# Optimization experiments

Hardware: AMD Instinct MI355X
Metric: run time of the kernel (lower is better)

The kernel has to match this reference:

```python
import jax, jax.numpy as jnp
import numpy as np

B, S, D, H = 2, 2048, 1024, 16
HD = D // H  # 64
ROPE_BASE = 10000.0


def setup_inputs() -> dict:
    key = jax.random.key(0)
    k1, k2, k3 = jax.random.split(key, 3)
    std = 1.0 / np.sqrt(D)
    x = jax.random.normal(k1, (B, S, D), dtype=jnp.float32)
    w_in = jax.random.normal(k2, (3 * D, D), dtype=jnp.float32) * std
    w_out = jax.random.normal(k3, (D, D), dtype=jnp.float32) * (std / np.sqrt(2.0))
    return {"x": x, "w_in": w_in, "w_out": w_out}


def _rope_cos_sin(seq_len, head_dim):
    inv_freq = 1.0 / (ROPE_BASE ** (jnp.arange(0, head_dim, 2, dtype=jnp.float32) / head_dim))
    t = jnp.arange(seq_len, dtype=jnp.float32)
    freqs = jnp.einsum("s,d->sd", t, inv_freq)          # [S, HD/2]
    emb = jnp.concatenate([freqs, freqs], axis=-1)       # [S, HD]
    return jnp.cos(emb)[None, :, None, :], jnp.sin(emb)[None, :, None, :]


def _rotate_half(x):
    x1, x2 = jnp.split(x, 2, axis=-1)
    return jnp.concatenate([-x2, x1], axis=-1)


def _apply_rope(x, cos, sin):
    return x * cos + _rotate_half(x) * sin


def reference(x, w_in, w_out):
    b, s, d = x.shape
    # fused QKV projection (no bias)
    qkv = x @ w_in.T                                      # [B, S, 3D]
    q, k, v = jnp.split(qkv, 3, axis=-1)
    q = q.reshape(b, s, H, HD)
    k = k.reshape(b, s, H, HD)
    v = v.reshape(b, s, H, HD)
    # rotary (offset = 0, no KV cache)
    cos, sin = _rope_cos_sin(s, HD)
    q = _apply_rope(q, cos, sin)
    k = _apply_rope(k, cos, sin)
    # causal SDPA, scale 1/sqrt(head_dim)
    scale = 1.0 / jnp.sqrt(jnp.asarray(HD, dtype=x.dtype))
    scores = jnp.einsum("bqhd,bkhd->bhqk", q, k) * scale  # [B, H, S, S]
    causal = jnp.tril(jnp.ones((s, s), dtype=bool))
    scores = jnp.where(causal, scores, jnp.asarray(-jnp.inf, dtype=scores.dtype))
    attn = jax.nn.softmax(scores, axis=-1)
    out = jnp.einsum("bhqk,bkhd->bqhd", attn, v).reshape(b, s, d)
    return out @ w_out.T
```

## Files before the change

kernel.cpp:

```cpp
#include <hip/hip_runtime.h>
#include <hip/hip_bf16.h>
#include <math.h>

#define NB 2
#define NS 2048
#define ND 1024
#define NH 16
#define HD 64
#define BS (NB*NS)
#define D3 (3*ND)
#define NT (NS/64)

typedef __bf16 bf16;
typedef __bf16 bf16x4 __attribute__((ext_vector_type(4)));
typedef __bf16 bf16x8 __attribute__((ext_vector_type(8)));
typedef float f32x4 __attribute__((ext_vector_type(4)));

#define MFMA16(a,b,c) __builtin_amdgcn_mfma_f32_16x16x32_bf16(a,b,c,0,0,0)

static __device__ inline f32x4 zero4() { f32x4 z; z[0]=0.f; z[1]=0.f; z[2]=0.f; z[3]=0.f; return z; }

__device__ __forceinline__ void gload_lds16(const bf16* g, bf16* l) {
    __builtin_amdgcn_global_load_lds(
        (__attribute__((address_space(1))) unsigned int*)g,
        (__attribute__((address_space(3))) unsigned int*)l, 16, 0, 0);
}

#define CVT1 (BS*ND/8)
#define CVT2 (D3*ND/8)
#define CVT3 (ND*ND/8)
#define CVTN (CVT1+CVT2+CVT3)
__global__ __launch_bounds__(256) void prep(
    const float* __restrict__ x, const float* __restrict__ w_in, const float* __restrict__ w_out,
    bf16* __restrict__ xb, bf16* __restrict__ winb, bf16* __restrict__ woutb,
    float2* __restrict__ csT)
{
    int i = blockIdx.x * 256 + threadIdx.x;
    if (i < CVTN) {
        const float* in; bf16* out; int j;
        if (i < CVT1)            { in = x;     out = xb;    j = i; }
        else if (i < CVT1+CVT2)  { in = w_in;  out = winb;  j = i - CVT1; }
        else                     { in = w_out; out = woutb; j = i - CVT1 - CVT2; }
        const float4* p = (const float4*)in;
        float4 a = p[j*2], b = p[j*2+1];
        bf16x8 o;
        o[0]=(bf16)a.x; o[1]=(bf16)a.y; o[2]=(bf16)a.z; o[3]=(bf16)a.w;
        o[4]=(bf16)b.x; o[5]=(bf16)b.y; o[6]=(bf16)b.z; o[7]=(bf16)b.w;
        ((bf16x8*)out)[j] = o;
    } else {
        int k = i - CVTN;
        int s = k >> 5, j = k & 31;
        float inv = __expf(-(float)j * (9.210340372f * 0.03125f));
        float ang = (float)s * inv;
        csT[k] = make_float2(cosf(ang), sinf(ang));
    }
}

template<int EPI>
__global__ __launch_bounds__(256) void gemm_bt(
    const bf16* __restrict__ A, const bf16* __restrict__ Bm,
    float* __restrict__ C, bf16* __restrict__ Qb, bf16* __restrict__ Kb, bf16* __restrict__ Vt,
    const float2* __restrict__ csT,
    int M, int N, int K)
{
    __shared__ bf16 As[2][128*64];
    __shared__ bf16 Bs[2][128*64];
    int t = threadIdx.x;
    int lane = t & 63, w = t >> 6;
    int wr = w >> 1, wc = w & 1;
    int lr = lane & 15, lg = lane >> 4;
    int m0 = blockIdx.y * 128, n0 = blockIdx.x * 128;

    int srow = lane >> 3;
    int schunk = (lane & 7) ^ srow;
    const bf16* gA = &A [(size_t)(m0 + w*32 + srow)*K + schunk*8];
    const bf16* gB = &Bm[(size_t)(n0 + w*32 + srow)*K + schunk*8];

    auto stage = [&](int kt) {
        int buf = kt & 1;
        bf16* lA = &As[buf][w*2048];
        bf16* lB = &Bs[buf][w*2048];
        int k0 = kt * 64;
        #pragma unroll
        for (int i=0;i<4;i++) {
            gload_lds16(gA + (size_t)(i*8)*K + k0, lA + i*512);
            gload_lds16(gB + (size_t)(i*8)*K + k0, lB + i*512);
        }
    };

    f32x4 acc[4][4];
    for (int m=0;m<4;m++) for (int n=0;n<4;n++) acc[m][n] = zero4();

    int nt = K >> 6;
    stage(0);
    stage(1);

    for (int kt = 0; kt < nt; kt++) {
        int cur = kt & 1;
        if (kt < nt-1) asm volatile("s_waitcnt vmcnt(8)" ::: "memory");
        else           asm volatile("s_waitcnt vmcnt(0)" ::: "memory");
        __builtin_amdgcn_s_barrier();
        __builtin_amdgcn_sched_barrier(0);

        bf16x8 af[2][4], bfr[2][4];
        #pragma unroll
        for (int ks=0;ks<2;ks++) {
            #pragma unroll
            for (int m=0;m<4;m++) {
                int row = wr*64 + m*16 + lr;
                af[ks][m] = *(const bf16x8*)&As[cur][row*64 + (((ks*4+lg) ^ (row&7))*8)];
            }
            #pragma unroll
            for (int n=0;n<4;n++) {
                int row = wc*64 + n*16 + lr;
                bfr[ks][n] = *(const bf16x8*)&Bs[cur][row*64 + (((ks*4+lg) ^ (row&7))*8)];
            }
        }
        asm volatile("s_waitcnt lgkmcnt(0)" ::: "memory");
        __builtin_amdgcn_sched_barrier(0);
        __builtin_amdgcn_s_barrier();
        __builtin_amdgcn_sched_barrier(0);

        if (kt + 2 < nt) stage(kt + 2);

        __builtin_amdgcn_s_setprio(1);
        #pragma unroll
        for (int ks=0;ks<2;ks++)
            #pragma unroll
            for (int m=0;m<4;m++)
                #pragma unroll
                for (int n=0;n<4;n++)
                    acc[m][n] = MFMA16(af[ks][m], bfr[ks][n], acc[m][n]);
        __builtin_amdgcn_s_setprio(0);
    }

    if (EPI == 0) {
        for (int m=0;m<4;m++) for (int n=0;n<4;n++) {
            int grow = m0 + wr*64 + m*16 + lg*4;
            int gcol = n0 + wc*64 + n*16 + lr;
            for (int r=0;r<4;r++)
                C[(size_t)(grow+r) * N + gcol] = acc[m][n][r];
        }
    } else {
        int which = n0 >> 10;
        if (which == 2) {
            for (int m=0;m<4;m++) for (int n=0;n<4;n++) {
                int grow = m0 + wr*64 + m*16 + lg*4;
                int gcol = n0 + wc*64 + n*16 + lr;
                int h = (gcol & 1023) >> 6, d = gcol & 63;
                int b = grow >> 11, s0 = grow & (NS-1);
                int shi = s0 & ~63, j = s0 & 63;
                int kp = ((j>>5)&1)*32 + ((j>>2)&3)*8 + ((j>>4)&1)*4;
                bf16x4 pv;
                for (int r=0;r<4;r++) pv[r] = (bf16)acc[m][n][r];
                *(bf16x4*)&Vt[((size_t)((b*NH + h)*HD + d))*NS + shi + kp] = pv;
            }
        } else {
            const float qs = 0.125f * 1.44269504f;
            bf16* dst = (which == 0) ? Qb : Kb;
            for (int m=0;m<4;m++) {
                int grow = m0 + wr*64 + m*16 + lg*4;
                #pragma unroll
                for (int n=0;n<2;n++) {
                    int gcol = n0 + wc*64 + n*16 + lr;
                    int h = (gcol & 1023) >> 6, j = gcol & 63;
                    #pragma unroll
                    for (int r=0;r<4;r++) {
                        int gm = grow + r;
                        int b = gm >> 11, s = gm & (NS-1);
                        float2 cs = csT[(s<<5)+j];
                        float x1 = acc[m][n][r], x2 = acc[m][n+2][r];
                        float y1 = x1*cs.x - x2*cs.y;
                        float y2 = x2*cs.x + x1*cs.y;
                        if (which == 0) { y1 *= qs; y2 *= qs; }
                        size_t off = ((size_t)((b*NH + h)*NS + s))*HD;
                        dst[off + j]      = (bf16)y1;
                        dst[off + j + 32] = (bf16)y2;
                    }
                }
            }
        }
    }
}

__global__ __launch_bounds__(256, 4) void attn_fwd(
    const bf16* __restrict__ Qb, const bf16* __restrict__ Kb, const bf16* __restrict__ Vp,
    bf16* __restrict__ AO)
{
    __shared__ bf16 Ks[2][64*64];
    __shared__ bf16 Vs[2][64*64];
    int t = threadIdx.x;
    int lane = t & 63, w = t >> 6;
    int lr = lane & 15, lg = lane >> 4;
    int wgid = blockIdx.x;
    int g = wgid >> 5;
    int qt = (g < 8) ? 31 - g : (g < 16) ? g - 8 : (g < 24) ? 39 - g : g - 16;
    int bh = wgid & 31;
    int b = bh >> 4, h = bh & 15;
    size_t base = (size_t)bh * NS * HD;
    int q0 = qt*64 + w*16;

    bf16x8 qf[2];
    #pragma unroll
    for (int c=0;c<2;c++)
        qf[c] = *(const bf16x8*)&Qb[base + (size_t)(q0+lr)*HD + c*32 + lg*8];

    bf16x8 onesf;
    #pragma unroll
    for (int i=0;i<8;i++) onesf[i] = (bf16)1.0f;

    f32x4 o[4];
    f32x4 lacc = zero4();
    #pragma unroll
    for (int n=0;n<4;n++) o[n] = zero4();
    f32x4 minit;
    minit[0] = -12.f; minit[1] = -12.f; minit[2] = -12.f; minit[3] = -12.f;

    int srow8 = lane >> 3;
    int schunk = (lane & 7) ^ srow8;
    int srcrow = w*8 + srow8;
    const bf16* gK = Kb + base + (size_t)srcrow*HD + schunk*8;
    const bf16* gV = Vp + base + (size_t)srcrow*NS + schunk*8;

    auto stage = [&](int kt) {
        int buf = kt & 1;
        int kv0 = kt * 64;
        #pragma unroll
        for (int i=0;i<2;i++) {
            gload_lds16(gK + (size_t)(kv0 + i*32)*HD, &Ks[buf][(i*32 + w*8)*64]);
            gload_lds16(gV + (size_t)(i*32)*NS + kv0, &Vs[buf][(i*32 + w*8)*64]);
        }
    };

    stage(0);
    if (qt > 0) stage(1);

    for (int kt = 0; kt <= qt; kt++) {
        int cur = kt & 1;
        bool last = (kt == qt);
        if (!last) asm volatile("s_waitcnt vmcnt(4)" ::: "memory");
        else       asm volatile("s_waitcnt vmcnt(0)" ::: "memory");
        __builtin_amdgcn_s_barrier();
        __builtin_amdgcn_sched_barrier(0);

        const bf16* ksb = &Ks[cur][0];
        const bf16* vsb = &Vs[cur][0];

        bf16x8 kf[4][2], vf[2][4];
        #pragma unroll
        for (int kb=0;kb<4;kb++) {
            int row = kb*16 + lr;
            kf[kb][0] = *(const bf16x8*)&ksb[row*64 + ((lg     ^ (row&7))*8)];
            kf[kb][1] = *(const bf16x8*)&ksb[row*64 + (((4+lg) ^ (row&7))*8)];
        }
        #pragma unroll
        for (int c=0;c<2;c++)
            #pragma unroll
            for (int n=0;n<4;n++) {
                int row = n*16 + lr;
                vf[c][n] = *(const bf16x8*)&vsb[row*64 + (((c*4+lg) ^ (row&7))*8)];
            }

        f32x4 sc[4];
        __builtin_amdgcn_s_setprio(1);
        #pragma unroll
        for (int kb=0;kb<4;kb++) {
            sc[kb] = MFMA16(kf[kb][0], qf[0], minit);
            sc[kb] = MFMA16(kf[kb][1], qf[1], sc[kb]);
        }
        __builtin_amdgcn_s_setprio(0);

        if (last) {
            int qi = q0 + lr;
            #pragma unroll
            for (int kb=0;kb<4;kb++)
                #pragma unroll
                for (int rr=0;rr<4;rr++)
                    if (kt*64 + kb*16 + lg*4 + rr > qi) sc[kb][rr] = -__builtin_inff();
        }

        bf16x8 pa[2];
        #pragma unroll
        for (int c=0;c<2;c++) {
            bf16x8 v;
            #pragma unroll
            for (int i=0;i<8;i++) v[i] = (bf16)exp2f(sc[c*2 + (i>>2)][i&3]);
            pa[c] = v;
        }

        asm volatile("s_waitcnt lgkmcnt(0)" ::: "memory");
        __builtin_amdgcn_sched_barrier(0);
        __builtin_amdgcn_s_barrier();
        __builtin_amdgcn_sched_barrier(0);

        if (kt + 2 <= qt) stage(kt + 2);

        __builtin_amdgcn_s_setprio(1);
        #pragma unroll
        for (int c=0;c<2;c++) {
            lacc = MFMA16(onesf, pa[c], lacc);
            #pragma unroll
            for (int n=0;n<4;n++)
                o[n] = MFMA16(vf[c][n], pa[c], o[n]);
        }
        __builtin_amdgcn_s_setprio(0);
    }

    float inv = 1.0f / lacc[0];
    int q = q0 + lr;
    #pragma unroll
    for (int n=0;n<4;n++) {
        bf16x4 ov;
        #pragma unroll
        for (int rr=0;rr<4;rr++) ov[rr] = (bf16)(o[n][rr] * inv);
        *(bf16x4*)&AO[((size_t)(b*NS + q)*NH + h)*HD + n*16 + lg*4] = ov;
    }
}

extern "C" void kernel_launch(void* const* d_in, const int* in_sizes, int n_in,
                              void* d_out, int out_size, void* d_ws, size_t ws_size,
                              hipStream_t stream) {
    const float* x     = (const float*)d_in[0];
    const float* w_in  = (const float*)d_in[1];
    const float* w_out = (const float*)d_in[2];
    float* out = (float*)d_out;

    char* p = (char*)d_ws;
    bf16* xb    = (bf16*)p; p += (size_t)BS*ND*2;
    bf16* winb  = (bf16*)p; p += (size_t)D3*ND*2;
    bf16* woutb = (bf16*)p; p += (size_t)ND*ND*2;
    bf16* Qb    = (bf16*)p; p += (size_t)NB*NH*NS*HD*2;
    bf16* Kb    = (bf16*)p; p += (size_t)NB*NH*NS*HD*2;
    bf16* Vp    = (bf16*)p; p += (size_t)NB*NH*NS*HD*2;
    bf16* AO    = (bf16*)p; p += (size_t)BS*ND*2;
    float2* csT = (float2*)p; p += (size_t)NS*32*8;

    prep<<<(CVTN + NS*32)/256, 256, 0, stream>>>(x, w_in, w_out, xb, winb, woutb, csT);
    gemm_bt<1><<<dim3(D3/128, BS/128), 256, 0, stream>>>(xb, winb, nullptr, Qb, Kb, Vp,
                                                         csT, BS, D3, ND);
    attn_fwd<<<NB*NH*NT, 256, 0, stream>>>(Qb, Kb, Vp, AO);
    gemm_bt<0><<<dim3(ND/128, BS/128), 256, 0, stream>>>(AO, woutb, out, nullptr, nullptr, nullptr,
                                                         nullptr, BS, ND, ND);
}
```

Measured before the change: 96.04 us.

## Use 256x256 eight-wave tile with ping-pong MFMA phases for QKV GEMM

Replaces the 128x128 QKV projection GEMM with a dedicated 512-thread kernel using 256x256 output tiles, so each loaded byte is reused across more MFMAs. The k-loop is split into four quadrant phases with barriers, priority bumps and staggered A/B prefetch, so LDS reads, global-to-LDS loads and MFMAs interleave across waves. The output GEMM is split into its own kernel. The grid for QKV shrinks to 12x16 blocks (192), which may underfill the GPU's compute units and raises register and LDS pressure (64KB LDS per block).

```diff
diff --git a/kernel.cpp b/kernel.cpp
--- a/kernel.cpp
+++ b/kernel.cpp
@@ -56,12 +56,189 @@
     }
 }
 
-template<int EPI>
-__global__ __launch_bounds__(256) void gemm_bt(
+__global__ __launch_bounds__(512, 2) void gemm8_qkv(
     const bf16* __restrict__ A, const bf16* __restrict__ Bm,
-    float* __restrict__ C, bf16* __restrict__ Qb, bf16* __restrict__ Kb, bf16* __restrict__ Vt,
-    const float2* __restrict__ csT,
-    int M, int N, int K)
+    bf16* __restrict__ Qb, bf16* __restrict__ Kb, bf16* __restrict__ Vt,
+    const float2* __restrict__ csT)
+{
+    __shared__ bf16 As[2][256*64];
+    __shared__ bf16 Bs[2][256*64];
+    int t = threadIdx.x;
+    int lane = t & 63, w = t >> 6;
+    int wr = w >> 2, wc = w & 3;
+    int lr = lane & 15, lg = lane >> 4;
+    int m0 = blockIdx.y * 256, n0 = blockIdx.x * 256;
+
+    int srow8 = lane >> 3;
+    int schunk = (lane & 7) ^ srow8;
+    const bf16* gA = A  + (size_t)(m0 + srow8)*ND + schunk*8;
+    const bf16* gB = Bm + (size_t)(n0 + srow8)*ND + schunk*8;
+
+    auto stageA = [&](int kt) {
+        int buf = kt & 1, k0 = kt*64;
+        #pragma unroll
+        for (int i=0;i<2;i++) {
+            int r0 = (w*2+i)*8;
+            gload_lds16(gA + (size_t)r0*ND + k0,       &As[buf][r0*64]);
+            gload_lds16(gA + (size_t)(128+r0)*ND + k0, &As[buf][(128+r0)*64]);
+        }
+    };
+    auto stageB = [&](int kt) {
+        int buf = kt & 1, k0 = kt*64;
+        #pragma unroll
+        for (int i=0;i<2;i++) {
+            int r0 = (w*2+i)*8;
+            gload_lds16(gB + (size_t)r0*ND + k0,       &Bs[buf][r0*64]);
+            gload_lds16(gB + (size_t)(128+r0)*ND + k0, &Bs[buf][(128+r0)*64]);
+        }
+    };
+
+    f32x4 acc[8][4];
+    #pragma unroll
+    for (int m=0;m<8;m++)
+        #pragma unroll
+        for (int n=0;n<4;n++) acc[m][n] = zero4();
+
+    bf16x8 af[4][2], bfr[4][2];
+
+    stageB(0); stageA(0); stageB(1); stageA(1);
+
+    for (int kt = 0; kt < 16; kt++) {
+        int cur = kt & 1;
+        const bf16* as = &As[cur][0];
+        const bf16* bs = &Bs[cur][0];
+        if (kt < 15) asm volatile("s_waitcnt vmcnt(8)" ::: "memory");
+        else         asm volatile("s_waitcnt vmcnt(0)" ::: "memory");
+        __builtin_amdgcn_s_barrier();
+        __builtin_amdgcn_sched_barrier(0);
+
+        #pragma unroll
+        for (int m=0;m<4;m++) {
+            int row = wr*128 + m*16 + lr;
+            af[m][0] = *(const bf16x8*)&as[row*64 + ((lg     ^ (row&7))*8)];
+            af[m][1] = *(const bf16x8*)&as[row*64 + (((4+lg) ^ (row&7))*8)];
+        }
+        #pragma unroll
+        for (int n=0;n<2;n++) {
+            int row = wc*64 + n*16 + lr;
+            bfr[n][0] = *(const bf16x8*)&bs[row*64 + ((lg     ^ (row&7))*8)];
+            bfr[n][1] = *(const bf16x8*)&bs[row*64 + (((4+lg) ^ (row&7))*8)];
+        }
+        asm volatile("s_waitcnt lgkmcnt(0)" ::: "memory");
+        __builtin_amdgcn_sched_barrier(0);
+        __builtin_amdgcn_s_setprio(1);
+        #pragma unroll
+        for (int ks=0;ks<2;ks++)
+            #pragma unroll
+            for (int m=0;m<4;m++)
+                #pragma unroll
+                for (int n=0;n<2;n++)
+                    acc[m][n] = MFMA16(af[m][ks], bfr[n][ks], acc[m][n]);
+        __builtin_amdgcn_s_setprio(0);
+        __builtin_amdgcn_s_barrier();
+        __builtin_amdgcn_sched_barrier(0);
+
+        #pragma unroll
+        for (int n=2;n<4;n++) {
+            int row = wc*64 + n*16 + lr;
+            bfr[n][0] = *(const bf16x8*)&bs[row*64 + ((lg     ^ (row&7))*8)];
+            bfr[n][1] = *(const bf16x8*)&bs[row*64 + (((4+lg) ^ (row&7))*8)];
+        }
+        asm volatile("s_waitcnt lgkmcnt(0)" ::: "memory");
+        __builtin_amdgcn_sched_barrier(0);
+        __builtin_amdgcn_s_setprio(1);
+        #pragma unroll
+        for (int ks=0;ks<2;ks++)
+            #pragma unroll
+            for (int m=0;m<4;m++)
+                #pragma unroll
+                for (int n=2;n<4;n++)
+                    acc[m][n] = MFMA16(af[m][ks], bfr[n][ks], acc[m][n]);
+        __builtin_amdgcn_s_setprio(0);
+        __builtin_amdgcn_s_barrier();
+        __builtin_amdgcn_sched_barrier(0);
+
+        if (kt + 2 < 16) stageB(kt + 2);
+        #pragma unroll
+        for (int m=0;m<4;m++) {
+            int row = wr*128 + (m+4)*16 + lr;
+            af[m][0] = *(const bf16x8*)&as[row*64 + ((lg     ^ (row&7))*8)];
+            af[m][1] = *(const bf16x8*)&as[row*64 + (((4+lg) ^ (row&7))*8)];
+        }
+        asm volatile("s_waitcnt lgkmcnt(0)" ::: "memory");
+        __builtin_amdgcn_sched_barrier(0);
+        __builtin_amdgcn_s_setprio(1);
+        #pragma unroll
+        for (int ks=0;ks<2;ks++)
+            #pragma unroll
+            for (int m=0;m<4;m++)
+                #pragma unroll
+                for (int n=0;n<2;n++)
+                    acc[m+4][n] = MFMA16(af[m][ks], bfr[n][ks], acc[m+4][n]);
+        __builtin_amdgcn_s_setprio(0);
+        __builtin_amdgcn_s_barrier();
+        __builtin_amdgcn_sched_barrier(0);
+
+        if (kt + 2 < 16) stageA(kt + 2);
+        __builtin_amdgcn_s_setprio(1);
+        #pragma unroll
+        for (int ks=0;ks<2;ks++)
+            #pragma unroll
+            for (int m=0;m<4;m++)
+                #pragma unroll
+                for (int n=2;n<4;n++)
+                    acc[m+4][n] = MFMA16(af[m][ks], bfr[n][ks], acc[m+4][n]);
+        __builtin_amdgcn_s_setprio(0);
+    }
+
+    int which = n0 >> 10;
+    if (which == 2) {
+        #pragma unroll
+        for (int m=0;m<8;m++)
+            #pragma unroll
+            for (int n=0;n<4;n++) {
+                int grow = m0 + wr*128 + m*16 + lg*4;
+                int gcol = n0 + wc*64 + n*16 + lr;
+                int h = (gcol & 1023) >> 6, d = gcol & 63;
+                int b = grow >> 11, s0 = grow & (NS-1);
+                int shi = s0 & ~63, j = s0 & 63;
+                int kp = ((j>>5)&1)*32 + ((j>>2)&3)*8 + ((j>>4)&1)*4;
+                bf16x4 pv;
+                #pragma unroll
+                for (int r=0;r<4;r++) pv[r] = (bf16)acc[m][n][r];
+                *(bf16x4*)&Vt[((size_t)((b*NH + h)*HD + d))*NS + shi + kp] = pv;
+            }
+    } else {
+        const float qs = 0.125f * 1.44269504f;
+        bf16* dst = (which == 0) ? Qb : Kb;
+        #pragma unroll
+        for (int m=0;m<8;m++) {
+            int grow = m0 + wr*128 + m*16 + lg*4;
+            #pragma unroll
+            for (int n=0;n<2;n++) {
+                int gcol = n0 + wc*64 + n*16 + lr;
+                int h = (gcol & 1023) >> 6, j = gcol & 63;
+                #pragma unroll
+                for (int r=0;r<4;r++) {
+                    int gm = grow + r;
+                    int b = gm >> 11, s = gm & (NS-1);
+                    float2 cs = csT[(s<<5)+j];
+                    float x1 = acc[m][n][r], x2 = acc[m][n+2][r];
+                    float y1 = x1*cs.x - x2*cs.y;
+                    float y2 = x2*cs.x + x1*cs.y;
+                    if (which == 0) { y1 *= qs; y2 *= qs; }
+                    size_t off = ((size_t)((b*NH + h)*NS + s))*HD;
+                    dst[off + j]      = (bf16)y1;
+                    dst[off + j + 32] = (bf16)y2;
+                }
+            }
+        }
+    }
+}
+
+__global__ __launch_bounds__(256) void gemm_out(
+    const bf16* __restrict__ A, const bf16* __restrict__ Bm,
+    float* __restrict__ C, int M, int N, int K)
 {
     __shared__ bf16 As[2][128*64];
     __shared__ bf16 Bs[2][128*64];
@@ -134,52 +311,11 @@
         __builtin_amdgcn_s_setprio(0);
     }
 
-    if (EPI == 0) {
-        for (int m=0;m<4;m++) for (int n=0;n<4;n++) {
-            int grow = m0 + wr*64 + m*16 + lg*4;
-            int gcol = n0 + wc*64 + n*16 + lr;
-            for (int r=0;r<4;r++)
-                C[(size_t)(grow+r) * N + gcol] = acc[m][n][r];
-        }
-    } else {
-        int which = n0 >> 10;
-        if (which == 2) {
-            for (int m=0;m<4;m++) for (int n=0;n<4;n++) {
-                int grow = m0 + wr*64 + m*16 + lg*4;
-                int gcol = n0 + wc*64 + n*16 + lr;
-                int h = (gcol & 1023) >> 6, d = gcol & 63;
-                int b = grow >> 11, s0 = grow & (NS-1);
-                int shi = s0 & ~63, j = s0 & 63;
-                int kp = ((j>>5)&1)*32 + ((j>>2)&3)*8 + ((j>>4)&1)*4;
-                bf16x4 pv;
-                for (int r=0;r<4;r++) pv[r] = (bf16)acc[m][n][r];
-                *(bf16x4*)&Vt[((size_t)((b*NH + h)*HD + d))*NS + shi + kp] = pv;
-            }
-        } else {
-            const float qs = 0.125f * 1.44269504f;
-            bf16* dst = (which == 0) ? Qb : Kb;
-            for (int m=0;m<4;m++) {
-                int grow = m0 + wr*64 + m*16 + lg*4;
-                #pragma unroll
-                for (int n=0;n<2;n++) {
-                    int gcol = n0 + wc*64 + n*16 + lr;
-                    int h = (gcol & 1023) >> 6, j = gcol & 63;
-                    #pragma unroll
-                    for (int r=0;r<4;r++) {
-                        int gm = grow + r;
-                        int b = gm >> 11, s = gm & (NS-1);
-                        float2 cs = csT[(s<<5)+j];
-                        float x1 = acc[m][n][r], x2 = acc[m][n+2][r];
-                        float y1 = x1*cs.x - x2*cs.y;
-                        float y2 = x2*cs.x + x1*cs.y;
-                        if (which == 0) { y1 *= qs; y2 *= qs; }
-                        size_t off = ((size_t)((b*NH + h)*NS + s))*HD;
-                        dst[off + j]      = (bf16)y1;
-                        dst[off + j + 32] = (bf16)y2;
-                    }
-                }
-            }
-        }
+    for (int m=0;m<4;m++) for (int n=0;n<4;n++) {
+        int grow = m0 + wr*64 + m*16 + lg*4;
+        int gcol = n0 + wc*64 + n*16 + lr;
+        for (int r=0;r<4;r++)
+            C[(size_t)(grow+r) * N + gcol] = acc[m][n][r];
     }
 }
 
@@ -336,9 +472,7 @@
     float2* csT = (float2*)p; p += (size_t)NS*32*8;
 
     prep<<<(CVTN + NS*32)/256, 256, 0, stream>>>(x, w_in, w_out, xb, winb, woutb, csT);
-    gemm_bt<1><<<dim3(D3/128, BS/128), 256, 0, stream>>>(xb, winb, nullptr, Qb, Kb, Vp,
-                                                         csT, BS, D3, ND);
+    gemm8_qkv<<<dim3(D3/256, BS/256), 512, 0, stream>>>(xb, winb, Qb, Kb, Vp, csT);
     attn_fwd<<<NB*NH*NT, 256, 0, stream>>>(Qb, Kb, Vp, AO);
-    gemm_bt<0><<<dim3(ND/128, BS/128), 256, 0, stream>>>(AO, woutb, out, nullptr, nullptr, nullptr,
-                                                         nullptr, BS, ND, ND);
-}
+    gemm_out<<<dim3(ND/128, BS/128), 256, 0, stream>>>(AO, woutb, out, BS, ND, ND);
+}
```

Measured after the change: 95.95 us, median of 2. About the same (-0.1%).

## Specialize QKV GEMM with 128x192 tiles and grouped B-fragment loading

Applied to the files above, without the earlier changes.

Splits the templated GEMM into a dedicated QKV kernel and a plain output-projection kernel. The QKV kernel uses 128x192 tiles (16x32=512 blocks instead of 24x32=768), with each wave owning 32 rows by all 192 columns. B fragments are loaded in three 64-column groups interleaved with MFMAs, and the next stage is issued mid-iteration. The aim is to raise arithmetic intensity and reduce wave-quantization tail effects. In exchange it uses more LDS and registers (launch bounds 256,2), and the RoPE/V-transpose epilogue is reindexed.

```diff
diff --git a/kernel.cpp b/kernel.cpp
--- a/kernel.cpp
+++ b/kernel.cpp
@@ -56,12 +56,141 @@
     }
 }
 
-template<int EPI>
-__global__ __launch_bounds__(256) void gemm_bt(
+__global__ __launch_bounds__(256, 2) void gemm_qkv(
     const bf16* __restrict__ A, const bf16* __restrict__ Bm,
-    float* __restrict__ C, bf16* __restrict__ Qb, bf16* __restrict__ Kb, bf16* __restrict__ Vt,
-    const float2* __restrict__ csT,
-    int M, int N, int K)
+    bf16* __restrict__ Qb, bf16* __restrict__ Kb, bf16* __restrict__ Vt,
+    const float2* __restrict__ csT)
+{
+    __shared__ bf16 As[2][128*64];
+    __shared__ bf16 Bs[2][192*64];
+    int t = threadIdx.x;
+    int lane = t & 63, w = t >> 6;
+    int lr = lane & 15, lg = lane >> 4;
+    int m0 = blockIdx.y * 128, n0 = blockIdx.x * 192;
+
+    int srow8 = lane >> 3;
+    int schunk = (lane & 7) ^ srow8;
+    const bf16* gA = A  + (size_t)(m0 + srow8)*ND + schunk*8;
+    const bf16* gB = Bm + (size_t)(n0 + srow8)*ND + schunk*8;
+
+    auto stage = [&](int kt) {
+        int buf = kt & 1, k0 = kt*64;
+        #pragma unroll
+        for (int i=0;i<4;i++) {
+            int r0 = w*32 + i*8;
+            gload_lds16(gA + (size_t)r0*ND + k0, &As[buf][r0*64]);
+        }
+        #pragma unroll
+        for (int i=0;i<6;i++) {
+            int r0 = w*48 + i*8;
+            gload_lds16(gB + (size_t)r0*ND + k0, &Bs[buf][r0*64]);
+        }
+    };
+
+    f32x4 acc[2][12];
+    #pragma unroll
+    for (int mm=0;mm<2;mm++)
+        #pragma unroll
+        for (int n=0;n<12;n++) acc[mm][n] = zero4();
+
+    bf16x8 af[2][2], bfr[4][2];
+
+    stage(0); stage(1);
+
+    for (int kt = 0; kt < 16; kt++) {
+        int cur = kt & 1;
+        const bf16* as = &As[cur][0];
+        const bf16* bs = &Bs[cur][0];
+        if (kt < 15) asm volatile("s_waitcnt vmcnt(10)" ::: "memory");
+        else         asm volatile("s_waitcnt vmcnt(0)" ::: "memory");
+        __builtin_amdgcn_s_barrier();
+        __builtin_amdgcn_sched_barrier(0);
+
+        #pragma unroll
+        for (int mm=0;mm<2;mm++) {
+            int row = w*32 + mm*16 + lr;
+            af[mm][0] = *(const bf16x8*)&as[row*64 + ((lg     ^ (row&7))*8)];
+            af[mm][1] = *(const bf16x8*)&as[row*64 + (((4+lg) ^ (row&7))*8)];
+        }
+
+        #pragma unroll
+        for (int g=0; g<3; g++) {
+            #pragma unroll
+            for (int nn=0;nn<4;nn++) {
+                int row = g*64 + nn*16 + lr;
+                bfr[nn][0] = *(const bf16x8*)&bs[row*64 + ((lg     ^ (row&7))*8)];
+                bfr[nn][1] = *(const bf16x8*)&bs[row*64 + (((4+lg) ^ (row&7))*8)];
+            }
+            asm volatile("s_waitcnt lgkmcnt(0)" ::: "memory");
+            __builtin_amdgcn_sched_barrier(0);
+            if (g == 2) {
+                __builtin_amdgcn_s_barrier();
+                __builtin_amdgcn_sched_barrier(0);
+                if (kt + 2 < 16) stage(kt + 2);
+            }
+            __builtin_amdgcn_s_setprio(1);
+            #pragma unroll
+            for (int ks=0;ks<2;ks++)
+                #pragma unroll
+                for (int mm=0;mm<2;mm++)
+                    #pragma unroll
+                    for (int nn=0;nn<4;nn++)
+                        acc[mm][g*4+nn] = MFMA16(af[mm][ks], bfr[nn][ks], acc[mm][g*4+nn]);
+            __builtin_amdgcn_s_setprio(0);
+        }
+    }
+
+    const float qs = 0.125f * 1.44269504f;
+    #pragma unroll
+    for (int a=0;a<3;a++) {
+        int colbase = n0 + a*64;
+        int which = colbase >> 10;
+        if (which == 2) {
+            #pragma unroll
+            for (int p=0;p<4;p++)
+                #pragma unroll
+                for (int mm=0;mm<2;mm++) {
+                    int gcol = colbase + p*16 + lr;
+                    int h = (gcol & 1023) >> 6, d = gcol & 63;
+                    int grow = m0 + w*32 + mm*16 + lg*4;
+                    int b = grow >> 11, s0 = grow & (NS-1);
+                    int shi = s0 & ~63, j = s0 & 63;
+                    int kp = ((j>>5)&1)*32 + ((j>>2)&3)*8 + ((j>>4)&1)*4;
+                    bf16x4 pv;
+                    #pragma unroll
+                    for (int r=0;r<4;r++) pv[r] = (bf16)acc[mm][a*4+p][r];
+                    *(bf16x4*)&Vt[((size_t)((b*NH + h)*HD + d))*NS + shi + kp] = pv;
+                }
+        } else {
+            bf16* dst = (which == 0) ? Qb : Kb;
+            #pragma unroll
+            for (int p=0;p<2;p++)
+                #pragma unroll
+                for (int mm=0;mm<2;mm++) {
+                    int gcol = colbase + p*16 + lr;
+                    int h = (gcol & 1023) >> 6, j = gcol & 63;
+                    int grow = m0 + w*32 + mm*16 + lg*4;
+                    #pragma unroll
+                    for (int r=0;r<4;r++) {
+                        int gm = grow + r;
+                        int b = gm >> 11, s = gm & (NS-1);
+                        float2 cs = csT[(s<<5)+j];
+                        float x1 = acc[mm][a*4+p][r], x2 = acc[mm][a*4+p+2][r];
+                        float y1 = x1*cs.x - x2*cs.y;
+                        float y2 = x2*cs.x + x1*cs.y;
+                        if (which == 0) { y1 *= qs; y2 *= qs; }
+                        size_t off = ((size_t)((b*NH + h)*NS + s))*HD;
+                        dst[off + j]      = (bf16)y1;
+                        dst[off + j + 32] = (bf16)y2;
+                    }
+                }
+        }
+    }
+}
+
+__global__ __launch_bounds__(256) void gemm_out(
+    const bf16* __restrict__ A, const bf16* __restrict__ Bm,
+    float* __restrict__ C, int M, int N, int K)
 {
     __shared__ bf16 As[2][128*64];
     __shared__ bf16 Bs[2][128*64];
@@ -134,52 +263,11 @@
         __builtin_amdgcn_s_setprio(0);
     }
 
-    if (EPI == 0) {
-        for (int m=0;m<4;m++) for (int n=0;n<4;n++) {
-            int grow = m0 + wr*64 + m*16 + lg*4;
-            int gcol = n0 + wc*64 + n*16 + lr;
-            for (int r=0;r<4;r++)
-                C[(size_t)(grow+r) * N + gcol] = acc[m][n][r];
-        }
-    } else {
-        int which = n0 >> 10;
-        if (which == 2) {
-            for (int m=0;m<4;m++) for (int n=0;n<4;n++) {
-                int grow = m0 + wr*64 + m*16 + lg*4;
-                int gcol = n0 + wc*64 + n*16 + lr;
-                int h = (gcol & 1023) >> 6, d = gcol & 63;
-                int b = grow >> 11, s0 = grow & (NS-1);
-                int shi = s0 & ~63, j = s0 & 63;
-                int kp = ((j>>5)&1)*32 + ((j>>2)&3)*8 + ((j>>4)&1)*4;
-                bf16x4 pv;
-                for (int r=0;r<4;r++) pv[r] = (bf16)acc[m][n][r];
-                *(bf16x4*)&Vt[((size_t)((b*NH + h)*HD + d))*NS + shi + kp] = pv;
-            }
-        } else {
-            const float qs = 0.125f * 1.44269504f;
-            bf16* dst = (which == 0) ? Qb : Kb;
-            for (int m=0;m<4;m++) {
-                int grow = m0 + wr*64 + m*16 + lg*4;
-                #pragma unroll
-                for (int n=0;n<2;n++) {
-                    int gcol = n0 + wc*64 + n*16 + lr;
-                    int h = (gcol & 1023) >> 6, j = gcol & 63;
-                    #pragma unroll
-                    for (int r=0;r<4;r++) {
-                        int gm = grow + r;
-                        int b = gm >> 11, s = gm & (NS-1);
-                        float2 cs = csT[(s<<5)+j];
-                        float x1 = acc[m][n][r], x2 = acc[m][n+2][r];
-                        float y1 = x1*cs.x - x2*cs.y;
-                        float y2 = x2*cs.x + x1*cs.y;
-                        if (which == 0) { y1 *= qs; y2 *= qs; }
-                        size_t off = ((size_t)((b*NH + h)*NS + s))*HD;
-                        dst[off + j]      = (bf16)y1;
-                        dst[off + j + 32] = (bf16)y2;
-                    }
-                }
-            }
-        }
+    for (int m=0;m<4;m++) for (int n=0;n<4;n++) {
+        int grow = m0 + wr*64 + m*16 + lg*4;
+        int gcol = n0 + wc*64 + n*16 + lr;
+        for (int r=0;r<4;r++)
+            C[(size_t)(grow+r) * N + gcol] = acc[m][n][r];
     }
 }
 
@@ -336,9 +424,7 @@
     float2* csT = (float2*)p; p += (size_t)NS*32*8;
 
     prep<<<(CVTN + NS*32)/256, 256, 0, stream>>>(x, w_in, w_out, xb, winb, woutb, csT);
-    gemm_bt<1><<<dim3(D3/128, BS/128), 256, 0, stream>>>(xb, winb, nullptr, Qb, Kb, Vp,
-                                                         csT, BS, D3, ND);
+    gemm_qkv<<<dim3(D3/192, BS/128), 256, 0, stream>>>(xb, winb, Qb, Kb, Vp, csT);
     attn_fwd<<<NB*NH*NT, 256, 0, stream>>>(Qb, Kb, Vp, AO);
-    gemm_bt<0><<<dim3(ND/128, BS/128), 256, 0, stream>>>(AO, woutb, out, nullptr, nullptr, nullptr,
-                                                         nullptr, BS, ND, ND);
-}
+    gemm_out<<<dim3(ND/128, BS/128), 256, 0, stream>>>(AO, woutb, out, BS, ND, ND);
+}
```

After: 91.50 us (median of 2 runs). 1.05x faster.
